# Optimization experiments

Hardware: AMD Instinct MI355X
Metric: run time of the kernel (lower is better)

## Reference

```python
import jax, jax.numpy as jnp
import numpy as np

B, P, E = 4, 1024, 768
S, H = 16, 64  # senses, sense_head_dim
EPS = 1e-5
NEG = -1e15


def setup_inputs() -> dict:
    key = jax.random.key(0)
    ks = jax.random.split(key, 3)
    x = jax.random.normal(ks[0], (B, P, E), dtype=jnp.float32)
    # causal mask: 1.0 where key_position <= position
    mask = jnp.tril(jnp.ones((P, P), dtype=jnp.float32))
    W = jax.random.normal(ks[1], (E, 2, S, H), dtype=jnp.float32) * 0.02
    b = jnp.zeros((2, S, H), dtype=jnp.float32)
    ln_scale = jnp.ones((S,), dtype=jnp.float32)
    ln_bias = jnp.zeros((S,), dtype=jnp.float32)
    return {"x": x, "mask": mask, "W": W, "b": b, "ln_scale": ln_scale, "ln_bias": ln_bias}


def reference(x, mask, W, b, ln_scale, ln_bias):
    # c_attn: [B,P,E] @ [E,2,S,H] -> [B,2,P,S,H]
    qk = jnp.einsum("bpe,eqsh->bqpsh", x, W) + b[None, :, None, :, :]
    q, k = qk[:, 0], qk[:, 1]            # [B,P,S,H]
    q = q * jax.lax.rsqrt(float(H))
    # attn scores over head_dim: [B,S,P,Kpos]
    scores = jnp.einsum("bpsh,bksh->bspk", q, k)
    scores = scores + (1.0 - mask)[None, None, :, :] * NEG
    w = jax.nn.softmax(scores, axis=-1)  # softmax over key_position
    # dropout: inference=True -> identity
    # LayerNorm over the Senses axis (axis=1)
    mu = jnp.mean(w, axis=1, keepdims=True)
    var = jnp.var(w, axis=1, keepdims=True)
    wn = (w - mu) * jax.lax.rsqrt(var + EPS)
    out = wn * ln_scale[None, :, None, None] + ln_bias[None, :, None, None]
    return out  # [B, senses, position, key_position]
```

## Files before the change

### kernel.cpp

```cpp
#include <hip/hip_runtime.h>
#include <hip/hip_bf16.h>
#include <math.h>


typedef __bf16 bf16_t;
typedef __bf16 bf16x4_t __attribute__((ext_vector_type(4)));
typedef __bf16 bf16x8_t __attribute__((ext_vector_type(8)));
typedef float  f32x4_t  __attribute__((ext_vector_type(4)));
typedef float  f32x16_t __attribute__((ext_vector_type(16)));

#define DEV __device__ __forceinline__
static constexpr float kLog2e = 1.4426950408889634f;

DEV void gload_lds16(const bf16_t* g, bf16_t* l) {
  __builtin_amdgcn_global_load_lds(
      (const __attribute__((address_space(1))) void*)g,
      (__attribute__((address_space(3))) void*)l, 16, 0, 0);
}

__global__ __launch_bounds__(256) void k_cvt_x(const float* __restrict__ x,
                                               bf16_t* __restrict__ xb) {
  size_t i = ((size_t)blockIdx.x * 256 + threadIdx.x) * 8;
  f32x4_t a = *(const f32x4_t*)(x + i);
  f32x4_t b = *(const f32x4_t*)(x + i + 4);
  bf16x8_t o = {(bf16_t)a[0], (bf16_t)a[1], (bf16_t)a[2], (bf16_t)a[3],
                (bf16_t)b[0], (bf16_t)b[1], (bf16_t)b[2], (bf16_t)b[3]};
  *(bf16x8_t*)(xb + i) = o;
}

__global__ __launch_bounds__(256) void k_tr_w(const float* __restrict__ W,
                                              bf16_t* __restrict__ Wt) {
  __shared__ float t[32][33];
  int n0 = blockIdx.x * 32, e0 = blockIdx.y * 32;
  int tx = threadIdx.x & 31, ty = threadIdx.x >> 5;
#pragma unroll
  for (int i = 0; i < 4; i++)
    t[ty + 8 * i][tx] = W[(size_t)(e0 + ty + 8 * i) * 2048 + n0 + tx];
  __syncthreads();
#pragma unroll
  for (int i = 0; i < 4; i++)
    Wt[(size_t)(n0 + ty + 8 * i) * 768 + e0 + tx] = (bf16_t)t[tx][ty + 8 * i];
}

__global__ __launch_bounds__(256) void k_proj(const bf16_t* __restrict__ xb,
                                              const bf16_t* __restrict__ Wt,
                                              const float* __restrict__ bias,
                                              bf16_t* __restrict__ q_ws,
                                              bf16_t* __restrict__ k_ws) {
  __shared__ bf16_t As[128 * 32];
  __shared__ bf16_t Bs[128 * 32];
  const int tid = threadIdx.x;
  const int lane = tid & 63;
  const int w = tid >> 6;
  const int m0 = blockIdx.y * 128;
  const int n0 = blockIdx.x * 128;
  const int mw = (w >> 1) * 64, nw = (w & 1) * 64;

  f32x4_t zz = {0.f, 0.f, 0.f, 0.f};
  f32x4_t acc[4][4];
#pragma unroll
  for (int mt = 0; mt < 4; mt++)
#pragma unroll
    for (int nt = 0; nt < 4; nt++) acc[mt][nt] = zz;

  for (int k0 = 0; k0 < 768; k0 += 32) {
    __syncthreads();
#pragma unroll
    for (int i = 0; i < 2; i++) {
      int cbase = w * 128 + i * 64;
      int c = cbase + lane;
      int r = c >> 2, q8 = c & 3;
      gload_lds16(xb + (size_t)(m0 + r) * 768 + k0 + q8 * 8, As + cbase * 8);
      gload_lds16(Wt + (size_t)(n0 + r) * 768 + k0 + q8 * 8, Bs + cbase * 8);
    }
    __syncthreads();
    bf16x8_t a[4], b[4];
#pragma unroll
    for (int mt = 0; mt < 4; mt++)
      a[mt] = *(const bf16x8_t*)(As + (mw + mt * 16 + (lane & 15)) * 32 + (lane >> 4) * 8);
#pragma unroll
    for (int nt = 0; nt < 4; nt++)
      b[nt] = *(const bf16x8_t*)(Bs + (nw + nt * 16 + (lane & 15)) * 32 + (lane >> 4) * 8);
#pragma unroll
    for (int mt = 0; mt < 4; mt++)
#pragma unroll
      for (int nt = 0; nt < 4; nt++)
        acc[mt][nt] = __builtin_amdgcn_mfma_f32_16x16x32_bf16(a[mt], b[nt], acc[mt][nt], 0, 0, 0);
  }

#pragma unroll
  for (int mt = 0; mt < 4; mt++) {
    int row0 = mw + mt * 16 + (lane >> 4) * 4;
#pragma unroll
    for (int nt = 0; nt < 4; nt++) {
      int col = nw + nt * 16 + (lane & 15);
      int n = n0 + col;
      int s = (n >> 6) & 15, h = n & 63, qk = n >> 10;
      float bv = bias[n];
#pragma unroll
      for (int j = 0; j < 4; j++) {
        int m = m0 + row0 + j;
        int bi = m >> 10, p = m & 1023;
        float v = acc[mt][nt][j] + bv;
        size_t off = ((size_t)(bi * 16 + s) * 1024 + p) * 64 + h;
        if (qk == 0) q_ws[off] = (bf16_t)(v * 0.125f);
        else         k_ws[off] = (bf16_t)v;
      }
    }
  }
}

__global__ __launch_bounds__(256) void k_sumexp(const bf16_t* __restrict__ q_ws,
                                                const bf16_t* __restrict__ k_ws,
                                                float* __restrict__ rl_ws) {
  const int tid = threadIdx.x, lane = tid & 63, w = tid >> 6;
  const int bs = blockIdx.y;
  const int r0 = blockIdx.x * 64 + w * 16;
  const size_t base = (size_t)bs * 65536;

  const bf16_t* qrow = q_ws + base + (size_t)(r0 + (lane & 15)) * 64 + (lane >> 4) * 8;
  bf16x8_t A0 = *(const bf16x8_t*)(qrow);
  bf16x8_t A1 = *(const bf16x8_t*)(qrow + 32);

  float sum[4] = {0.f, 0.f, 0.f, 0.f};
  const int ktmax = (r0 + 15) >> 4;
  for (int kt = 0; kt <= ktmax; kt++) {
    const bf16_t* krow = k_ws + base + (size_t)(kt * 16 + (lane & 15)) * 64 + (lane >> 4) * 8;
    bf16x8_t B0 = *(const bf16x8_t*)(krow);
    bf16x8_t B1 = *(const bf16x8_t*)(krow + 32);
    f32x4_t z = {0.f, 0.f, 0.f, 0.f};
    f32x4_t sc = __builtin_amdgcn_mfma_f32_16x16x32_bf16(A0, B0, z, 0, 0, 0);
    sc = __builtin_amdgcn_mfma_f32_16x16x32_bf16(A1, B1, sc, 0, 0, 0);
    int col = kt * 16 + (lane & 15);
#pragma unroll
    for (int j = 0; j < 4; j++) {
      int row = r0 + (lane >> 4) * 4 + j;
      float e = (col <= row) ? exp2f(sc[j] * kLog2e) : 0.f;
      sum[j] += e;
    }
  }
#pragma unroll
  for (int j = 0; j < 4; j++)
#pragma unroll
    for (int msk = 1; msk < 16; msk <<= 1) sum[j] += __shfl_xor(sum[j], msk, 64);
  if ((lane & 15) == 0) {
#pragma unroll
    for (int j = 0; j < 4; j++)
      rl_ws[(size_t)bs * 1024 + r0 + (lane >> 4) * 4 + j] = 1.0f / sum[j];
  }
}

__global__ __launch_bounds__(512, 4) void k_final(const bf16_t* __restrict__ q_ws,
                                                  const bf16_t* __restrict__ k_ws,
                                                  const float* __restrict__ rl_ws,
                                                  const float* __restrict__ ln_scale,
                                                  const float* __restrict__ ln_bias,
                                                  float* __restrict__ out) {
  const int tid = threadIdx.x, lane = tid & 63, w = tid >> 6;
  const int raw = blockIdx.x;
  const int swz = (raw & 7) * 512 + (raw >> 3);
  const int bb = swz >> 10, pb = (swz >> 5) & 31, kb = swz & 31;
  const int pbase = pb * 32, kbase = kb * 32;

  if (kbase > pbase + 31) {
#pragma unroll
    for (int it = 0; it < 8; it++) {
      int idx = it * 512 + tid;
      int s = idx >> 8, rem = idx & 255;
      int pl = rem >> 3, kq = (rem & 7) * 4;
      float bv = ln_bias[s];
      f32x4_t v = {bv, bv, bv, bv};
      __builtin_nontemporal_store(
          v, (f32x4_t*)(out + ((size_t)(bb * 16 + s) * 1024 + pbase + pl) * 1024 + kbase + kq));
    }
    return;
  }

  __shared__ float part_sum[8][1024];
  __shared__ float part_ssq[8][1024];
  __shared__ float mu_lds[1024];
  __shared__ float rs_lds[1024];
  __shared__ float rl_lds[16][32];

  const int col = lane & 31, hi = lane >> 5;
  const int kcol = kbase + col;

  {
    int s = tid >> 5, pr = tid & 31;
    rl_lds[s][pr] = rl_ws[(size_t)(bb * 16 + s) * 1024 + pbase + pr];
  }

  f32x16_t c[2];
#pragma unroll
  for (int sp = 0; sp < 2; sp++)
#pragma unroll
    for (int j = 0; j < 16; j++) c[sp][j] = 0.f;

#pragma unroll
  for (int sp = 0; sp < 2; sp++) {
    int s = w * 2 + sp;
    size_t base = (size_t)(bb * 16 + s) * 65536;
    const bf16_t* qrow = q_ws + base + (size_t)(pbase + col) * 64 + hi * 8;
    const bf16_t* krow = k_ws + base + (size_t)kcol * 64 + hi * 8;
    bf16x8_t qa[4], kv[4];
#pragma unroll
    for (int t = 0; t < 4; t++) {
      qa[t] = *(const bf16x8_t*)(qrow + t * 16);
      kv[t] = *(const bf16x8_t*)(krow + t * 16);
    }
#pragma unroll
    for (int t = 0; t < 4; t++)
      c[sp] = __builtin_amdgcn_mfma_f32_32x32x16_bf16(qa[t], kv[t], c[sp], 0, 0, 0);
  }

  __syncthreads();

  float sum_p[16], ssq_p[16];
#pragma unroll
  for (int j = 0; j < 16; j++) { sum_p[j] = 0.f; ssq_p[j] = 0.f; }
#pragma unroll
  for (int sp = 0; sp < 2; sp++) {
    int s = w * 2 + sp;
#pragma unroll
    for (int j = 0; j < 16; j++) {
      int prl = (j & 3) + 8 * (j >> 2) + 4 * hi;
      float wv = (kcol <= pbase + prl) ? exp2f(c[sp][j] * kLog2e) * rl_lds[s][prl] : 0.f;
      c[sp][j] = wv;
      sum_p[j] += wv;
      ssq_p[j] = fmaf(wv, wv, ssq_p[j]);
    }
  }

#pragma unroll
  for (int j = 0; j < 16; j++) {
    int prl = (j & 3) + 8 * (j >> 2) + 4 * hi;
    int cell = prl * 32 + col;
    part_sum[w][cell] = sum_p[j];
    part_ssq[w][cell] = ssq_p[j];
  }
  __syncthreads();

  if (tid < 256) {
    int q4 = tid * 4;
    f32x4_t s4 = {0.f, 0.f, 0.f, 0.f}, qq = {0.f, 0.f, 0.f, 0.f};
#pragma unroll
    for (int i = 0; i < 8; i++) {
      s4 += *(const f32x4_t*)&part_sum[i][q4];
      qq += *(const f32x4_t*)&part_ssq[i][q4];
    }
    f32x4_t m = s4 * 0.0625f;
    f32x4_t var = qq * 0.0625f - m * m;
    f32x4_t r;
#pragma unroll
    for (int e = 0; e < 4; e++) r[e] = rsqrtf(var[e] + 1e-5f);
    *(f32x4_t*)&mu_lds[q4] = m;
    *(f32x4_t*)&rs_lds[q4] = r;
  }
  __syncthreads();

  float mu[16], rs[16];
#pragma unroll
  for (int j = 0; j < 16; j++) {
    int prl = (j & 3) + 8 * (j >> 2) + 4 * hi;
    int cell = prl * 32 + col;
    mu[j] = mu_lds[cell];
    rs[j] = rs_lds[cell];
  }

#pragma unroll
  for (int sp = 0; sp < 2; sp++) {
    int s = w * 2 + sp;
    float scl = ln_scale[s], bi = ln_bias[s];
    size_t hb = ((size_t)(bb * 16 + s) * 1024 + pbase) * 1024 + kbase;
#pragma unroll
    for (int j = 0; j < 16; j++) {
      int prl = (j & 3) + 8 * (j >> 2) + 4 * hi;
      __builtin_nontemporal_store((c[sp][j] - mu[j]) * rs[j] * scl + bi,
                                  &out[hb + (size_t)prl * 1024 + col]);
    }
  }
}

extern "C" void kernel_launch(void* const* d_in, const int* in_sizes, int n_in,
                              void* d_out, int out_size, void* d_ws, size_t ws_size,
                              hipStream_t stream) {
  (void)in_sizes; (void)n_in; (void)out_size; (void)ws_size;
  const float* x        = (const float*)d_in[0];
  const float* W        = (const float*)d_in[2];
  const float* bias     = (const float*)d_in[3];
  const float* ln_scale = (const float*)d_in[4];
  const float* ln_bias  = (const float*)d_in[5];
  float* out = (float*)d_out;

  char* ws = (char*)d_ws;
  bf16_t* q_ws = (bf16_t*)ws;
  bf16_t* k_ws = (bf16_t*)(ws + 8388608);
  float*  rl_ws = (float*)(ws + 16777216);
  bf16_t* xb   = (bf16_t*)(ws + 17039360);
  bf16_t* Wt   = (bf16_t*)(ws + 23330816);

  k_cvt_x<<<dim3(1536), 256, 0, stream>>>(x, xb);
  k_tr_w <<<dim3(64, 24), 256, 0, stream>>>(W, Wt);
  k_proj <<<dim3(16, 32), 256, 0, stream>>>(xb, Wt, bias, q_ws, k_ws);
  k_sumexp<<<dim3(16, 64), 256, 0, stream>>>(q_ws, k_ws, rl_ws);
  k_final<<<dim3(4096), 512, 0, stream>>>(q_ws, k_ws, rl_ws, ln_scale, ln_bias, out);
}
```

Measured before the change: 165.3 us.

## Use 32x32 MFMA tiles in sumexp and LDS atomics for sense LayerNorm reduction

The softmax-denominator kernel now has each wave handle 32 query rows with 32x32x16 MFMA tiles. Each lane owns a single query row, so the cross-lane sum collapses to one shuffle, and the grid is halved. In the final kernel, the 8-way partial-sum buffers and the separate reduction pass are replaced by LDS atomicAdd into a single sum and sum-of-squares buffer. This shrinks shared memory use and removes one barrier plus a serial reduction step, in exchange for atomic contention on LDS cells.

```diff
diff --git a/kernel.cpp b/kernel.cpp
--- a/kernel.cpp
+++ b/kernel.cpp
@@ -115,39 +115,37 @@
                                                 float* __restrict__ rl_ws) {
   const int tid = threadIdx.x, lane = tid & 63, w = tid >> 6;
   const int bs = blockIdx.y;
-  const int r0 = blockIdx.x * 64 + w * 16;
+  const int r0 = blockIdx.x * 128 + w * 32;
   const size_t base = (size_t)bs * 65536;
-
-  const bf16_t* qrow = q_ws + base + (size_t)(r0 + (lane & 15)) * 64 + (lane >> 4) * 8;
-  bf16x8_t A0 = *(const bf16x8_t*)(qrow);
-  bf16x8_t A1 = *(const bf16x8_t*)(qrow + 32);
-
-  float sum[4] = {0.f, 0.f, 0.f, 0.f};
-  const int ktmax = (r0 + 15) >> 4;
+  const int col = lane & 31, hi = lane >> 5;
+  const int p = r0 + col;
+
+  bf16x8_t qb[4];
+  const bf16_t* qrow = q_ws + base + (size_t)p * 64 + hi * 8;
+#pragma unroll
+  for (int t = 0; t < 4; t++) qb[t] = *(const bf16x8_t*)(qrow + t * 16);
+
+  float sum = 0.f;
+  const int ktmax = r0 >> 5;
   for (int kt = 0; kt <= ktmax; kt++) {
-    const bf16_t* krow = k_ws + base + (size_t)(kt * 16 + (lane & 15)) * 64 + (lane >> 4) * 8;
-    bf16x8_t B0 = *(const bf16x8_t*)(krow);
-    bf16x8_t B1 = *(const bf16x8_t*)(krow + 32);
-    f32x4_t z = {0.f, 0.f, 0.f, 0.f};
-    f32x4_t sc = __builtin_amdgcn_mfma_f32_16x16x32_bf16(A0, B0, z, 0, 0, 0);
-    sc = __builtin_amdgcn_mfma_f32_16x16x32_bf16(A1, B1, sc, 0, 0, 0);
-    int col = kt * 16 + (lane & 15);
-#pragma unroll
-    for (int j = 0; j < 4; j++) {
-      int row = r0 + (lane >> 4) * 4 + j;
-      float e = (col <= row) ? exp2f(sc[j] * kLog2e) : 0.f;
-      sum[j] += e;
-    }
-  }
-#pragma unroll
-  for (int j = 0; j < 4; j++)
-#pragma unroll
-    for (int msk = 1; msk < 16; msk <<= 1) sum[j] += __shfl_xor(sum[j], msk, 64);
-  if ((lane & 15) == 0) {
-#pragma unroll
-    for (int j = 0; j < 4; j++)
-      rl_ws[(size_t)bs * 1024 + r0 + (lane >> 4) * 4 + j] = 1.0f / sum[j];
-  }
+    const bf16_t* krow = k_ws + base + (size_t)(kt * 32 + col) * 64 + hi * 8;
+    bf16x8_t ka[4];
+#pragma unroll
+    for (int t = 0; t < 4; t++) ka[t] = *(const bf16x8_t*)(krow + t * 16);
+    f32x16_t c;
+#pragma unroll
+    for (int j = 0; j < 16; j++) c[j] = 0.f;
+#pragma unroll
+    for (int t = 0; t < 4; t++)
+      c = __builtin_amdgcn_mfma_f32_32x32x16_bf16(ka[t], qb[t], c, 0, 0, 0);
+#pragma unroll
+    for (int j = 0; j < 16; j++) {
+      int kk = kt * 32 + (j & 3) + 8 * (j >> 2) + 4 * hi;
+      if (kk <= p) sum += exp2f(c[j] * kLog2e);
+    }
+  }
+  sum += __shfl_xor(sum, 32, 64);
+  if (hi == 0) rl_ws[(size_t)bs * 1024 + p] = 1.0f / sum;
 }
 
 __global__ __launch_bounds__(512, 4) void k_final(const bf16_t* __restrict__ q_ws,
@@ -176,10 +174,8 @@
     return;
   }
 
-  __shared__ float part_sum[8][1024];
-  __shared__ float part_ssq[8][1024];
-  __shared__ float mu_lds[1024];
-  __shared__ float rs_lds[1024];
+  __shared__ float part_sum[1024];
+  __shared__ float part_ssq[1024];
   __shared__ float rl_lds[16][32];
 
   const int col = lane & 31, hi = lane >> 5;
@@ -188,7 +184,10 @@
   {
     int s = tid >> 5, pr = tid & 31;
     rl_lds[s][pr] = rl_ws[(size_t)(bb * 16 + s) * 1024 + pbase + pr];
-  }
+    part_sum[tid] = 0.f; part_sum[tid + 256] = 0.f;
+    part_ssq[tid] = 0.f; part_ssq[tid + 256] = 0.f;
+  }
+  if (tid < 256) { part_sum[tid + 768] = 0.f; part_ssq[tid + 768] = 0.f; }
 
   f32x16_t c[2];
 #pragma unroll
@@ -230,31 +229,12 @@
       ssq_p[j] = fmaf(wv, wv, ssq_p[j]);
     }
   }
-
 #pragma unroll
   for (int j = 0; j < 16; j++) {
     int prl = (j & 3) + 8 * (j >> 2) + 4 * hi;
     int cell = prl * 32 + col;
-    part_sum[w][cell] = sum_p[j];
-    part_ssq[w][cell] = ssq_p[j];
-  }
-  __syncthreads();
-
-  if (tid < 256) {
-    int q4 = tid * 4;
-    f32x4_t s4 = {0.f, 0.f, 0.f, 0.f}, qq = {0.f, 0.f, 0.f, 0.f};
-#pragma unroll
-    for (int i = 0; i < 8; i++) {
-      s4 += *(const f32x4_t*)&part_sum[i][q4];
-      qq += *(const f32x4_t*)&part_ssq[i][q4];
-    }
-    f32x4_t m = s4 * 0.0625f;
-    f32x4_t var = qq * 0.0625f - m * m;
-    f32x4_t r;
-#pragma unroll
-    for (int e = 0; e < 4; e++) r[e] = rsqrtf(var[e] + 1e-5f);
-    *(f32x4_t*)&mu_lds[q4] = m;
-    *(f32x4_t*)&rs_lds[q4] = r;
+    atomicAdd(&part_sum[cell], sum_p[j]);
+    atomicAdd(&part_ssq[cell], ssq_p[j]);
   }
   __syncthreads();
 
@@ -263,8 +243,9 @@
   for (int j = 0; j < 16; j++) {
     int prl = (j & 3) + 8 * (j >> 2) + 4 * hi;
     int cell = prl * 32 + col;
-    mu[j] = mu_lds[cell];
-    rs[j] = rs_lds[cell];
+    float m = part_sum[cell] * 0.0625f;
+    mu[j] = m;
+    rs[j] = rsqrtf(part_ssq[cell] * 0.0625f - m * m + 1e-5f);
   }
 
 #pragma unroll
@@ -302,6 +283,6 @@
   k_cvt_x<<<dim3(1536), 256, 0, stream>>>(x, xb);
   k_tr_w <<<dim3(64, 24), 256, 0, stream>>>(W, Wt);
   k_proj <<<dim3(16, 32), 256, 0, stream>>>(xb, Wt, bias, q_ws, k_ws);
-  k_sumexp<<<dim3(16, 64), 256, 0, stream>>>(q_ws, k_ws, rl_ws);
+  k_sumexp<<<dim3(8, 64), 256, 0, stream>>>(q_ws, k_ws, rl_ws);
   k_final<<<dim3(4096), 512, 0, stream>>>(q_ws, k_ws, rl_ws, ln_scale, ln_bias, out);
 }
```

Result: slower. 368.0 us (+122.6%).
